# Kernel tuning notes

Measured on AMD Instinct MI355X. Metric: run time of the kernel, lower is better.

The kernel has to match this reference:

```python
import jax, jax.numpy as jnp
import numpy as np

# Static problem sizes (uniform graphs for jit-friendliness)
B = 64          # number of hypergraphs in the batch
N_PER = 32      # shape-nodes per hypergraph (num_nodes_hgraph, uniform)
D_ID = 256      # shape_id_dim
D_MULT = 64     # shape_multiplicity_dim
LATENT = 512    # latent_dim
D_NODE = D_ID + D_MULT           # 320
FEAT = 3 * D_NODE + LATENT       # 1472, MLP input dim
HID = 2 * FEAT                   # 2944
NUM_ATOMS = 11                   # 1 + feature_sizes['num_atoms']
VOCAB_ID, VOCAB_MULT = 100, 20


def setup_inputs() -> dict:
    key = jax.random.key(0)
    ks = jax.random.split(key, 11)
    s1 = 1.0 / np.sqrt(FEAT)
    s2 = 1.0 / np.sqrt(HID)
    s3 = 1.0 / np.sqrt(FEAT)
    return {
        "shape_node_idx": jax.random.randint(ks[0], (B * N_PER,), 0, VOCAB_ID),
        "shape_node_mult": jax.random.randint(ks[1], (B * N_PER,), 0, VOCAB_MULT),
        "z_graph": jax.random.normal(ks[2], (B, LATENT), jnp.float32),
        "id_emb": jax.random.normal(ks[3], (VOCAB_ID, D_ID), jnp.float32) * 0.02,
        "mult_emb": jax.random.normal(ks[4], (VOCAB_MULT, D_MULT), jnp.float32) * 0.02,
        "W1": jax.random.normal(ks[5], (FEAT, HID), jnp.float32) * s1,
        "b1": jnp.zeros((HID,), jnp.float32),
        "W2": jax.random.normal(ks[6], (HID, FEAT), jnp.float32) * s2,
        "b2": jnp.zeros((FEAT,), jnp.float32),
        "W3": jax.random.normal(ks[7], (FEAT, NUM_ATOMS), jnp.float32) * s3,
        "b3": jnp.zeros((NUM_ATOMS,), jnp.float32),
    }


def reference(shape_node_idx, shape_node_mult, z_graph, id_emb, mult_emb,
              W1, b1, W2, b2, W3, b3):
    # Node features: concat of shape-id and multiplicity embeddings -> [B, n, d_node]
    x = jnp.concatenate([id_emb[shape_node_idx], mult_emb[shape_node_mult]], axis=-1)
    x = x.reshape(B, N_PER, D_NODE)

    # Per-graph segment aggregation (node_aggregation='mean') -> [B, d_node]
    agg = x.mean(axis=1)

    # All intra-graph node pairs (block-diagonal edge pattern), edge (i, j):
    # input = [x_i, x_j, z_graph, agg] broadcast to [B, n, n, FEAT]
    xi = jnp.broadcast_to(x[:, :, None, :], (B, N_PER, N_PER, D_NODE))
    xj = jnp.broadcast_to(x[:, None, :, :], (B, N_PER, N_PER, D_NODE))
    zg = jnp.broadcast_to(z_graph[:, None, None, :], (B, N_PER, N_PER, LATENT))
    ag = jnp.broadcast_to(agg[:, None, None, :], (B, N_PER, N_PER, D_NODE))
    feat = jnp.concatenate([xi, xj, zg, ag], axis=-1)  # [B, n, n, FEAT]

    # MLP [FEAT, 2*FEAT, FEAT, NUM_ATOMS] with ReLU activations
    h = jax.nn.relu(jnp.einsum('bijf,fh->bijh', feat, W1) + b1)
    h = jax.nn.relu(jnp.einsum('bijh,hf->bijf', h, W2) + b2)
    logits = jnp.einsum('bijf,fa->bija', h, W3) + b3  # [B, n, n, A]

    # _to_symmetric: average each edge value with its transpose
    logits = 0.5 * (logits + jnp.swapaxes(logits, 1, 2))

    # Flattened per-edge logits (matches sparse COO value order: row-major pairs)
    return logits.reshape(B * N_PER * N_PER, NUM_ATOMS)
```

## Files before the change

### kernel.cpp

```cpp
#include <hip/hip_runtime.h>
#include <stdint.h>

#define NBG   64
#define NPER  32
#define DNODE 320
#define FEAT  1472
#define HIDN  2944
#define FEATP 1536
#define NA    11
#define NROWS 2048
#define MEDGE 65536

typedef __attribute__((ext_vector_type(8))) short    bf16x8;
typedef __attribute__((ext_vector_type(4))) float    fv4;
typedef __attribute__((ext_vector_type(4))) unsigned uiv4;

__device__ __forceinline__ unsigned short f2bf(float f) {
  unsigned u = __builtin_bit_cast(unsigned, f);
  u += 0x7fffu + ((u >> 16) & 1u);
  return (unsigned short)(u >> 16);
}
__device__ __forceinline__ float bf2f(unsigned short h) {
  unsigned u = ((unsigned)h) << 16;
  return __builtin_bit_cast(float, u);
}
__device__ __forceinline__ unsigned cvt_pk_bf16(float lo, float hi) {
  unsigned r;
  asm("v_cvt_pk_bf16_f32 %0, %1, %2" : "=v"(r) : "v"(lo), "v"(hi));
  return r;
}
__device__ __forceinline__ void gload_lds16(const void* g, void* l) {
  __builtin_amdgcn_global_load_lds((const __attribute__((address_space(1))) void*)g,
                                   (__attribute__((address_space(3))) void*)l, 16, 0, 0);
}

__global__ void k_transpose_bf16(const float* __restrict__ src, unsigned short* __restrict__ dst,
                                 int K, int N, int Npad) {
  __shared__ float tile[64][65];
  int k0 = blockIdx.x * 64, n0 = blockIdx.y * 64;
  int r = threadIdx.x >> 2, cb = (threadIdx.x & 3) * 16;
  const float* srow = src + (size_t)(k0 + r) * N + n0 + cb;
#pragma unroll
  for (int c = 0; c < 16; ++c) {
    int n = n0 + cb + c;
    tile[r][cb + c] = (n < N) ? srow[c] : 0.f;
  }
  __syncthreads();
  unsigned short* drow = dst + (size_t)(n0 + r) * K + k0 + cb;
#pragma unroll
  for (int c = 0; c < 16; ++c) drow[c] = f2bf(tile[cb + c][r]);
}

__global__ void k_embed(const int* __restrict__ idx, const int* __restrict__ mlt,
                        const float* __restrict__ id_emb, const float* __restrict__ mult_emb,
                        unsigned short* __restrict__ xb) {
  int t = blockIdx.x, c = threadIdx.x;
  int iv = idx[t], mv = mlt[t];
  xb[t * DNODE + c] = f2bf(id_emb[iv * 256 + c]);
  if (c < 64) xb[t * DNODE + 256 + c] = f2bf(mult_emb[mv * 64 + c]);
}

__global__ void k_agg(const unsigned short* __restrict__ xb, float* __restrict__ agg) {
  int b = blockIdx.x;
  for (int d = threadIdx.x; d < DNODE; d += 256) {
    float s = 0.f;
    for (int i = 0; i < NPER; ++i) s += bf2f(xb[(b * NPER + i) * DNODE + d]);
    agg[b * DNODE + d] = s * (1.f / 32.f);
  }
}

__global__ void k_za(const float* __restrict__ z, const float* __restrict__ agg,
                     unsigned short* __restrict__ za) {
  int b = blockIdx.x;
  for (int c = threadIdx.x; c < 832; c += 256) {
    unsigned short v = 0;
    if (b < NBG) v = (c < 512) ? f2bf(z[b * 512 + c]) : f2bf(agg[b * DNODE + (c - 512)]);
    za[b * 832 + c] = v;
  }
}

__global__ void k_gemm1(const unsigned short* __restrict__ A, int sA, int Mrows,
                        const unsigned short* __restrict__ W1T, int kOff, int Ksteps,
                        float* __restrict__ C, const float* __restrict__ bias) {
  __shared__ alignas(16) unsigned short Als[128 * 32];
  __shared__ alignas(16) unsigned short Bls[128 * 32];
  int bx = blockIdx.x;
  int mt = bx / 23, nc = bx - mt * 23;
  int m0 = mt * 128, n0 = nc * 128;
  int tid = threadIdx.x, lane = tid & 63, w = tid >> 6;

  fv4 acc[4][4] = {};
  for (int kt = 0; kt < Ksteps; ++kt) {
    int k0 = kt * 32;
    __syncthreads();
#pragma unroll
    for (int q = 0; q < 2; ++q) {
      int seg = w * 2 + q;
      int row = seg * 16 + (lane >> 2);
      int col = (lane & 3) * 8;
      gload_lds16(A + (size_t)(m0 + row) * sA + k0 + col, &Als[seg * 512]);
      gload_lds16(W1T + (size_t)(n0 + row) * FEAT + kOff + k0 + col, &Bls[seg * 512]);
    }
    __syncthreads();
    bf16x8 aF[4], bF[4];
#pragma unroll
    for (int mf = 0; mf < 4; ++mf)
      aF[mf] = *(const bf16x8*)&Als[((w >> 1) * 64 + mf * 16 + (lane & 15)) * 32 + (lane >> 4) * 8];
#pragma unroll
    for (int nf = 0; nf < 4; ++nf)
      bF[nf] = *(const bf16x8*)&Bls[((w & 1) * 64 + nf * 16 + (lane & 15)) * 32 + (lane >> 4) * 8];
#pragma unroll
    for (int mf = 0; mf < 4; ++mf)
#pragma unroll
      for (int nf = 0; nf < 4; ++nf)
        acc[mf][nf] = __builtin_amdgcn_mfma_f32_16x16x32_bf16(aF[mf], bF[nf], acc[mf][nf], 0, 0, 0);
  }
  int mq = (w >> 1) * 64, nq = (w & 1) * 64;
#pragma unroll
  for (int mf = 0; mf < 4; ++mf)
#pragma unroll
    for (int nf = 0; nf < 4; ++nf) {
      int n = n0 + nq + nf * 16 + (lane & 15);
      float bv = bias ? bias[n] : 0.f;
#pragma unroll
      for (int r = 0; r < 4; ++r) {
        int m = m0 + mq + mf * 16 + (lane >> 4) * 4 + r;
        if (m < Mrows) C[(size_t)m * HIDN + n] = acc[mf][nf][r] + bv;
      }
    }
}

__global__ void k_pq(float* __restrict__ P1, const float* __restrict__ Q) {
  int r = blockIdx.x;
  const float* q = Q + (size_t)(r >> 5) * HIDN;
  float* p = P1 + (size_t)r * HIDN;
  for (int n = threadIdx.x; n < HIDN; n += 256) p[n] += q[n];
}

__global__ void k_zero(float* __restrict__ p, int n) {
  int i = blockIdx.x * 256 + threadIdx.x;
  if (i < n) p[i] = 0.f;
}

__global__ __launch_bounds__(256, 3)
void k_gemm2(const float* __restrict__ PQ1, const float* __restrict__ P2,
             const unsigned short* __restrict__ W2T,
             const float* __restrict__ b2, const float* __restrict__ W3,
             float* __restrict__ Lraw) {
  __shared__ alignas(16) unsigned char LB[26624];
  int bx = blockIdx.x;
  int mt = bx / 12, nc = bx - mt * 12;
  int m0 = mt * 128, n0 = nc * 128;
  int tid = threadIdx.x, lane = tid & 63, w = tid >> 6;
  int bG = m0 >> 10;
  int i0 = (m0 >> 5) & 31;
  int ks = lane >> 4;
  int r  = lane & 15;

  const int swcolB = ((lane & 3) ^ ((lane >> 3) & 3)) * 8;
  const int swcolP = (((lane >> 1) & 3) ^ ((lane >> 3) & 3)) * 8 + (lane & 1) * 4;

  auto STAGEB = [&](int kt, int buf) {
#pragma unroll
    for (int q = 0; q < 2; ++q) {
      int seg = w * 2 + q;
      int row = seg * 16 + (lane >> 2);
      gload_lds16(W2T + (size_t)(n0 + row) * HIDN + kt * 32 + swcolB,
                  LB + buf * 8192 + seg * 1024);
    }
  };
  auto STAGESRC = [&](int kt, int buf) {
    gload_lds16(P2 + (size_t)(bG * NPER + 8 * w + (lane >> 3)) * HIDN + kt * 32 + swcolP,
                LB + 16384 + buf * 4096 + w * 1024);
    if (w == 0)
      gload_lds16(PQ1 + (size_t)(bG * NPER + i0 + (lane >> 3)) * HIDN + kt * 32 + (lane & 7) * 4,
                  LB + 24576 + buf * 1024);
  };

  fv4 acc[4][4] = {};

  STAGEB(0, 0);
  STAGESRC(0, 0);
  __syncthreads();

  for (int kt = 0; kt < 92; ++kt) {
    int cur = kt & 1, nxt = cur ^ 1;
    if (kt < 91) { STAGEB(kt + 1, nxt); STAGESRC(kt + 1, nxt); }

    const unsigned char* Bb = LB + cur * 8192;
    const unsigned char* Pb = LB + 16384 + cur * 4096;
    const unsigned char* Qb = LB + 24576 + cur * 1024;

    int il0 = (w >> 1) * 2;
    int psw = (ks ^ (r & 3)) * 32;
    fv4 q0[2], q1[2], p0[2], p1[2];
#pragma unroll
    for (int h = 0; h < 2; ++h) {
      q0[h] = *(const fv4*)(Qb + il0 * 128 + ks * 32 + h * 16);
      q1[h] = *(const fv4*)(Qb + (il0 + 1) * 128 + ks * 32 + h * 16);
      p0[h] = *(const fv4*)(Pb + r * 128 + psw + h * 16);
      p1[h] = *(const fv4*)(Pb + (16 + r) * 128 + psw + h * 16);
    }
    bf16x8 bF[4];
#pragma unroll
    for (int nf = 0; nf < 4; ++nf) {
      int brow = (w & 1) * 64 + nf * 16 + r;
      int slot = ks ^ ((brow >> 1) & 3);
      bF[nf] = *(const bf16x8*)(Bb + brow * 64 + slot * 16);
    }

    bf16x8 aF[4];
#pragma unroll
    for (int mf = 0; mf < 4; ++mf) {
      fv4 s0 = (mf & 2 ? q1[0] : q0[0]) + (mf & 1 ? p1[0] : p0[0]);
      fv4 s1 = (mf & 2 ? q1[1] : q0[1]) + (mf & 1 ? p1[1] : p0[1]);
      uiv4 u;
      u[0] = cvt_pk_bf16(fmaxf(s0[0], 0.f), fmaxf(s0[1], 0.f));
      u[1] = cvt_pk_bf16(fmaxf(s0[2], 0.f), fmaxf(s0[3], 0.f));
      u[2] = cvt_pk_bf16(fmaxf(s1[0], 0.f), fmaxf(s1[1], 0.f));
      u[3] = cvt_pk_bf16(fmaxf(s1[2], 0.f), fmaxf(s1[3], 0.f));
      aF[mf] = __builtin_bit_cast(bf16x8, u);
    }

#pragma unroll
    for (int mf = 0; mf < 4; ++mf)
#pragma unroll
      for (int nf = 0; nf < 4; ++nf)
        acc[mf][nf] = __builtin_amdgcn_mfma_f32_16x16x32_bf16(aF[mf], bF[nf], acc[mf][nf], 0, 0, 0);
    __syncthreads();
  }

  float* red = (float*)LB;
  int nq = (w & 1) * 64;
#pragma unroll
  for (int mf = 0; mf < 4; ++mf) {
    float s[4][NA];
#pragma unroll
    for (int rr = 0; rr < 4; ++rr)
#pragma unroll
      for (int a = 0; a < NA; ++a) s[rr][a] = 0.f;
#pragma unroll
    for (int nf = 0; nf < 4; ++nf) {
      int n = n0 + nq + nf * 16 + r;
      if (n < FEAT) {
        float bv = b2[n];
        float w3r[NA];
#pragma unroll
        for (int a = 0; a < NA; ++a) w3r[a] = W3[n * NA + a];
#pragma unroll
        for (int rr = 0; rr < 4; ++rr) {
          float h = fmaxf(acc[mf][nf][rr] + bv, 0.f);
#pragma unroll
          for (int a = 0; a < NA; ++a) s[rr][a] += h * w3r[a];
        }
      }
    }
#pragma unroll
    for (int off = 1; off < 16; off <<= 1)
#pragma unroll
      for (int rr = 0; rr < 4; ++rr)
#pragma unroll
        for (int a = 0; a < NA; ++a) s[rr][a] += __shfl_xor(s[rr][a], off, 64);
    int a = r;
    if (a < NA) {
#pragma unroll
      for (int rr = 0; rr < 4; ++rr)
        red[w * 704 + (mf * 16 + ks * 4 + rr) * NA + a] = s[rr][a];
    }
  }
  __syncthreads();
  for (int e = tid; e < 128 * NA; e += 256) {
    int row = e / NA, a = e - row * NA;
    int wr = row >> 6, rr = row & 63;
    float v = red[(wr * 2 + 0) * 704 + rr * NA + a] + red[(wr * 2 + 1) * 704 + rr * NA + a];
    atomicAdd(&Lraw[(size_t)(m0 + row) * NA + a], v);
  }
}

__global__ void k_sym(const float* __restrict__ Lraw, const float* __restrict__ b3,
                      float* __restrict__ out) {
  int e = blockIdx.x * 256 + threadIdx.x;
  if (e >= MEDGE * NA) return;
  int m = e / NA, a = e - m * NA;
  int msw = (m & ~1023) | ((m & 31) << 5) | ((m >> 5) & 31);
  out[e] = 0.5f * (Lraw[e] + Lraw[(size_t)msw * NA + a]) + b3[a];
}

extern "C" void kernel_launch(void* const* d_in, const int* in_sizes, int n_in,
                              void* d_out, int out_size, void* d_ws, size_t ws_size,
                              hipStream_t stream) {
  const int*   idx      = (const int*)d_in[0];
  const int*   mlt      = (const int*)d_in[1];
  const float* z        = (const float*)d_in[2];
  const float* id_emb   = (const float*)d_in[3];
  const float* mult_emb = (const float*)d_in[4];
  const float* W1       = (const float*)d_in[5];
  const float* b1       = (const float*)d_in[6];
  const float* W2       = (const float*)d_in[7];
  const float* b2       = (const float*)d_in[8];
  const float* W3       = (const float*)d_in[9];
  const float* b3       = (const float*)d_in[10];
  float* out = (float*)d_out;

  uint8_t* ws = (uint8_t*)d_ws;
  size_t o = 0;
  auto alloc = [&](size_t bytes) { size_t r = o; o += (bytes + 255) & ~(size_t)255; return r; };
  size_t oW1T = alloc((size_t)HIDN * FEAT * 2);
  size_t oW2T = alloc((size_t)FEATP * HIDN * 2);
  size_t oXB  = alloc((size_t)NROWS * DNODE * 2);
  size_t oZA  = alloc((size_t)128 * 832 * 2);
  size_t oAG  = alloc((size_t)NBG * DNODE * 4);
  size_t oP1  = alloc((size_t)NROWS * HIDN * 4);
  size_t oP2  = alloc((size_t)NROWS * HIDN * 4);
  size_t oQ   = alloc((size_t)NBG * HIDN * 4);
  size_t oLR  = alloc((size_t)MEDGE * NA * 4);
  if (ws_size < o) return;

  unsigned short* W1T = (unsigned short*)(ws + oW1T);
  unsigned short* W2T = (unsigned short*)(ws + oW2T);
  unsigned short* xb  = (unsigned short*)(ws + oXB);
  unsigned short* za  = (unsigned short*)(ws + oZA);
  float* agg = (float*)(ws + oAG);
  float* P1  = (float*)(ws + oP1);
  float* P2  = (float*)(ws + oP2);
  float* Qm  = (float*)(ws + oQ);
  float* LR  = (float*)(ws + oLR);

  k_transpose_bf16<<<dim3(FEAT / 64, HIDN / 64), 256, 0, stream>>>(W1, W1T, FEAT, HIDN, HIDN);
  k_transpose_bf16<<<dim3(HIDN / 64, FEATP / 64), 256, 0, stream>>>(W2, W2T, HIDN, FEAT, FEATP);
  k_embed<<<NROWS, 256, 0, stream>>>(idx, mlt, id_emb, mult_emb, xb);
  k_agg<<<NBG, 256, 0, stream>>>(xb, agg);
  k_za<<<128, 256, 0, stream>>>(z, agg, za);
  k_gemm1<<<16 * 23, 256, 0, stream>>>(xb, DNODE, NROWS, W1T, 0, 10, P1, nullptr);
  k_gemm1<<<16 * 23, 256, 0, stream>>>(xb, DNODE, NROWS, W1T, 320, 10, P2, nullptr);
  k_gemm1<<<1 * 23, 256, 0, stream>>>(za, 832, NBG, W1T, 640, 26, Qm, b1);
  k_pq<<<NROWS, 256, 0, stream>>>(P1, Qm);
  k_zero<<<(MEDGE * NA + 255) / 256, 256, 0, stream>>>(LR, MEDGE * NA);
  k_gemm2<<<512 * 12, 256, 0, stream>>>(P1, P2, W2T, b2, W3, LR);
  k_sym<<<(MEDGE * NA + 255) / 256, 256, 0, stream>>>(LR, b3, out);
}
```

Before: 1.318 ms.

## Materialize bf16 edge activations and replace atomics with per-column-tile partial sums

Adds a path that precomputes the relu(P1+P2) layer-1 activations for all edges as a bf16 matrix, so the second GEMM streams plain bf16 tiles instead of building them from fp32 sums inside the loop. The atomicAdd reduction is replaced by per-column-tile partial logits, which the symmetrization kernel sums; this also drops the zeroing kernel. The code picks a tier based on available workspace. Materializing the full 65536x2944 bf16 matrix adds a large amount of extra memory traffic, and the partial-sum buffer is twelve times larger than before.

New measurement: 1.317 ms. Within noise of the previous version (-0.0%).

```diff
diff --git a/kernel.cpp b/kernel.cpp
--- a/kernel.cpp
+++ b/kernel.cpp
@@ -142,11 +142,127 @@
   if (i < n) p[i] = 0.f;
 }
 
+__global__ void k_build_A(const float* __restrict__ PQ1, const float* __restrict__ P2,
+                          unsigned short* __restrict__ Abf) {
+  int bi = blockIdx.x;
+  int b = bi >> 5;
+  const float* qrow = PQ1 + (size_t)bi * HIDN;
+  const float* pbase = P2 + (size_t)(b * NPER) * HIDN;
+  unsigned short* abase = Abf + (size_t)bi * NPER * HIDN;
+  for (int j = 0; j < NPER; ++j) {
+    const float* prow = pbase + (size_t)j * HIDN;
+    unsigned short* arow = abase + (size_t)j * HIDN;
+    for (int kc = threadIdx.x; kc < HIDN / 8; kc += 256) {
+      fv4 q0 = *(const fv4*)(qrow + kc * 8);
+      fv4 q1 = *(const fv4*)(qrow + kc * 8 + 4);
+      fv4 p0 = *(const fv4*)(prow + kc * 8);
+      fv4 p1 = *(const fv4*)(prow + kc * 8 + 4);
+      fv4 s0 = q0 + p0, s1 = q1 + p1;
+      uiv4 u;
+      u[0] = cvt_pk_bf16(fmaxf(s0[0], 0.f), fmaxf(s0[1], 0.f));
+      u[1] = cvt_pk_bf16(fmaxf(s0[2], 0.f), fmaxf(s0[3], 0.f));
+      u[2] = cvt_pk_bf16(fmaxf(s1[0], 0.f), fmaxf(s1[1], 0.f));
+      u[3] = cvt_pk_bf16(fmaxf(s1[2], 0.f), fmaxf(s1[3], 0.f));
+      *(uiv4*)(arow + kc * 8) = u;
+    }
+  }
+}
+
+__global__ __launch_bounds__(256, 3)
+void k_gemm2m(const unsigned short* __restrict__ A, const unsigned short* __restrict__ W2T,
+              const float* __restrict__ b2, const float* __restrict__ W3,
+              float* __restrict__ LRp) {
+  __shared__ alignas(16) unsigned char LB[16384];
+  unsigned short* Als = (unsigned short*)LB;
+  unsigned short* Bls = (unsigned short*)(LB + 8192);
+  int raw = blockIdx.x;
+  int bx = (raw & 7) * 768 + (raw >> 3);
+  int mt = bx / 12, nc = bx - mt * 12;
+  int m0 = mt * 128, n0 = nc * 128;
+  int tid = threadIdx.x, lane = tid & 63, w = tid >> 6;
+  int r = lane & 15, ks = lane >> 4;
+
+  fv4 acc[4][4] = {};
+  for (int kt = 0; kt < 92; ++kt) {
+    int k0 = kt * 32;
+    __syncthreads();
+#pragma unroll
+    for (int q = 0; q < 2; ++q) {
+      int seg = w * 2 + q;
+      int row = seg * 16 + (lane >> 2);
+      int col = (lane & 3) * 8;
+      gload_lds16(A + (size_t)(m0 + row) * HIDN + k0 + col, &Als[seg * 512]);
+      gload_lds16(W2T + (size_t)(n0 + row) * HIDN + k0 + col, &Bls[seg * 512]);
+    }
+    __syncthreads();
+    bf16x8 aF[4], bF[4];
+#pragma unroll
+    for (int mf = 0; mf < 4; ++mf)
+      aF[mf] = *(const bf16x8*)&Als[((w >> 1) * 64 + mf * 16 + r) * 32 + ks * 8];
+#pragma unroll
+    for (int nf = 0; nf < 4; ++nf)
+      bF[nf] = *(const bf16x8*)&Bls[((w & 1) * 64 + nf * 16 + r) * 32 + ks * 8];
+#pragma unroll
+    for (int mf = 0; mf < 4; ++mf)
+#pragma unroll
+      for (int nf = 0; nf < 4; ++nf)
+        acc[mf][nf] = __builtin_amdgcn_mfma_f32_16x16x32_bf16(aF[mf], bF[nf], acc[mf][nf], 0, 0, 0);
+  }
+  __syncthreads();
+
+  float* red = (float*)LB;
+  int nq = (w & 1) * 64;
+#pragma unroll
+  for (int mf = 0; mf < 4; ++mf) {
+    float s[4][NA];
+#pragma unroll
+    for (int rr = 0; rr < 4; ++rr)
+#pragma unroll
+      for (int a = 0; a < NA; ++a) s[rr][a] = 0.f;
+#pragma unroll
+    for (int nf = 0; nf < 4; ++nf) {
+      int n = n0 + nq + nf * 16 + r;
+      if (n < FEAT) {
+        float bv = b2[n];
+        float w3r[NA];
+#pragma unroll
+        for (int a = 0; a < NA; ++a) w3r[a] = W3[n * NA + a];
+#pragma unroll
+        for (int rr = 0; rr < 4; ++rr) {
+          float h = fmaxf(acc[mf][nf][rr] + bv, 0.f);
+#pragma unroll
+          for (int a = 0; a < NA; ++a) s[rr][a] += h * w3r[a];
+        }
+      }
+    }
+#pragma unroll
+    for (int off = 1; off < 16; off <<= 1)
+#pragma unroll
+      for (int rr = 0; rr < 4; ++rr)
+#pragma unroll
+        for (int a = 0; a < NA; ++a) s[rr][a] += __shfl_xor(s[rr][a], off, 64);
+    int a = r;
+    if (a < NA) {
+#pragma unroll
+      for (int rr = 0; rr < 4; ++rr)
+        red[w * 704 + (mf * 16 + ks * 4 + rr) * NA + a] = s[rr][a];
+    }
+  }
+  __syncthreads();
+  for (int e = tid; e < 128 * NA; e += 256) {
+    int row = e / NA, a = e - row * NA;
+    int wr = row >> 6, rr = row & 63;
+    float v = red[(wr * 2 + 0) * 704 + rr * NA + a] + red[(wr * 2 + 1) * 704 + rr * NA + a];
+    LRp[(size_t)nc * (MEDGE * NA) + (size_t)(m0 + row) * NA + a] = v;
+  }
+}
+
+template <bool PARTIAL>
 __global__ __launch_bounds__(256, 3)
 void k_gemm2(const float* __restrict__ PQ1, const float* __restrict__ P2,
              const unsigned short* __restrict__ W2T,
              const float* __restrict__ b2, const float* __restrict__ W3,
-             float* __restrict__ Lraw) {
+             float* __restrict__ Lout) {
   __shared__ alignas(16) unsigned char LB[26624];
   int bx = blockIdx.x;
   int mt = bx / 12, nc = bx - mt * 12;
@@ -229,6 +345,7 @@
         acc[mf][nf] = __builtin_amdgcn_mfma_f32_16x16x32_bf16(aF[mf], bF[nf], acc[mf][nf], 0, 0, 0);
     __syncthreads();
   }
+  __syncthreads();
 
   float* red = (float*)LB;
   int nq = (w & 1) * 64;
@@ -273,17 +390,25 @@
     int row = e / NA, a = e - row * NA;
     int wr = row >> 6, rr = row & 63;
     float v = red[(wr * 2 + 0) * 704 + rr * NA + a] + red[(wr * 2 + 1) * 704 + rr * NA + a];
-    atomicAdd(&Lraw[(size_t)(m0 + row) * NA + a], v);
-  }
-}
-
-__global__ void k_sym(const float* __restrict__ Lraw, const float* __restrict__ b3,
+    if (PARTIAL)
+      Lout[(size_t)nc * (MEDGE * NA) + (size_t)(m0 + row) * NA + a] = v;
+    else
+      atomicAdd(&Lout[(size_t)(m0 + row) * NA + a], v);
+  }
+}
+
+template <int NS>
+__global__ void k_sym(const float* __restrict__ LRp, const float* __restrict__ b3,
                       float* __restrict__ out) {
   int e = blockIdx.x * 256 + threadIdx.x;
   if (e >= MEDGE * NA) return;
   int m = e / NA, a = e - m * NA;
   int msw = (m & ~1023) | ((m & 31) << 5) | ((m >> 5) & 31);
-  out[e] = 0.5f * (Lraw[e] + Lraw[(size_t)msw * NA + a]) + b3[a];
+  float s = 0.f;
+#pragma unroll
+  for (int t = 0; t < NS; ++t)
+    s += LRp[(size_t)t * (MEDGE * NA) + e] + LRp[(size_t)t * (MEDGE * NA) + (size_t)msw * NA + a];
+  out[e] = 0.5f * s + b3[a];
 }
 
 extern "C" void kernel_launch(void* const* d_in, const int* in_sizes, int n_in,
@@ -313,8 +438,13 @@
   size_t oP1  = alloc((size_t)NROWS * HIDN * 4);
   size_t oP2  = alloc((size_t)NROWS * HIDN * 4);
   size_t oQ   = alloc((size_t)NBG * HIDN * 4);
-  size_t oLR  = alloc((size_t)MEDGE * NA * 4);
-  if (ws_size < o) return;
+  size_t oLRp = alloc((size_t)12 * MEDGE * NA * 4);
+  size_t needB = o;
+  size_t oA   = alloc((size_t)MEDGE * HIDN * 2);
+  size_t needA = o;
+  size_t needC = oLRp + (((size_t)MEDGE * NA * 4 + 255) & ~(size_t)255);
+  if (ws_size < needC) return;
+  int tier = (ws_size >= needA) ? 0 : (ws_size >= needB ? 1 : 2);
 
   unsigned short* W1T = (unsigned short*)(ws + oW1T);
   unsigned short* W2T = (unsigned short*)(ws + oW2T);
@@ -324,7 +454,8 @@
   float* P1  = (float*)(ws + oP1);
   float* P2  = (float*)(ws + oP2);
   float* Qm  = (float*)(ws + oQ);
-  float* LR  = (float*)(ws + oLR);
+  float* LRp = (float*)(ws + oLRp);
+  unsigned short* Abf = (unsigned short*)(ws + oA);
 
   k_transpose_bf16<<<dim3(FEAT / 64, HIDN / 64), 256, 0, stream>>>(W1, W1T, FEAT, HIDN, HIDN);
   k_transpose_bf16<<<dim3(HIDN / 64, FEATP / 64), 256, 0, stream>>>(W2, W2T, HIDN, FEAT, FEATP);
@@ -335,7 +466,17 @@
   k_gemm1<<<16 * 23, 256, 0, stream>>>(xb, DNODE, NROWS, W1T, 320, 10, P2, nullptr);
   k_gemm1<<<1 * 23, 256, 0, stream>>>(za, 832, NBG, W1T, 640, 26, Qm, b1);
   k_pq<<<NROWS, 256, 0, stream>>>(P1, Qm);
-  k_zero<<<(MEDGE * NA + 255) / 256, 256, 0, stream>>>(LR, MEDGE * NA);
-  k_gemm2<<<512 * 12, 256, 0, stream>>>(P1, P2, W2T, b2, W3, LR);
-  k_sym<<<(MEDGE * NA + 255) / 256, 256, 0, stream>>>(LR, b3, out);
-}
+
+  if (tier == 0) {
+    k_build_A<<<NROWS, 256, 0, stream>>>(P1, P2, Abf);
+    k_gemm2m<<<512 * 12, 256, 0, stream>>>(Abf, W2T, b2, W3, LRp);
+    k_sym<12><<<(MEDGE * NA + 255) / 256, 256, 0, stream>>>(LRp, b3, out);
+  } else if (tier == 1) {
+    k_gemm2<true><<<512 * 12, 256, 0, stream>>>(P1, P2, W2T, b2, W3, LRp);
+    k_sym<12><<<(MEDGE * NA + 255) / 256, 256, 0, stream>>>(LRp, b3, out);
+  } else {
+    k_zero<<<(MEDGE * NA + 255) / 256, 256, 0, stream>>>(LRp, MEDGE * NA);
+    k_gemm2<false><<<512 * 12, 256, 0, stream>>>(P1, P2, W2T, b2, W3, LRp);
+    k_sym<1><<<(MEDGE * NA + 255) / 256, 256, 0, stream>>>(LRp, b3, out);
+  }
+}
```

## Widen gemm2 N-tile to 256, swizzle block order, write partial logits instead of atomics

Applied to the files above, without the earlier changes.

The fused second GEMM now computes 128x256 tiles per block (8 N-fragments per wave), which halves how often the P/Q activation sources are restaged and rebuilt per output column. Block indices are remapped across 8 groups to change the cache locality of co-resident blocks. When the workspace is large enough, each N-chunk writes its partial W3 projection to a separate slice, and the symmetrization kernel sums the six slices, removing the zeroing pass and the atomics. The larger accumulator set raises register and LDS pressure and lowers occupancy to 2 blocks per CU.

Result: faster. 1.154 ms (-12.4%).

```diff
diff --git a/kernel.cpp b/kernel.cpp
--- a/kernel.cpp
+++ b/kernel.cpp
@@ -142,15 +142,17 @@
   if (i < n) p[i] = 0.f;
 }
 
-__global__ __launch_bounds__(256, 3)
+template <bool PARTIAL>
+__global__ __launch_bounds__(256, 2)
 void k_gemm2(const float* __restrict__ PQ1, const float* __restrict__ P2,
              const unsigned short* __restrict__ W2T,
              const float* __restrict__ b2, const float* __restrict__ W3,
-             float* __restrict__ Lraw) {
-  __shared__ alignas(16) unsigned char LB[26624];
-  int bx = blockIdx.x;
-  int mt = bx / 12, nc = bx - mt * 12;
-  int m0 = mt * 128, n0 = nc * 128;
+             float* __restrict__ Lout) {
+  __shared__ alignas(16) unsigned char LB[43008];
+  int raw = blockIdx.x;
+  int bx = (raw & 7) * 384 + (raw >> 3);
+  int mt = bx / 6, nc2 = bx - mt * 6;
+  int m0 = mt * 128, n0 = nc2 * 256;
   int tid = threadIdx.x, lane = tid & 63, w = tid >> 6;
   int bG = m0 >> 10;
   int i0 = (m0 >> 5) & 31;
@@ -162,22 +164,22 @@
 
   auto STAGEB = [&](int kt, int buf) {
 #pragma unroll
-    for (int q = 0; q < 2; ++q) {
-      int seg = w * 2 + q;
+    for (int q = 0; q < 4; ++q) {
+      int seg = w * 4 + q;
       int row = seg * 16 + (lane >> 2);
       gload_lds16(W2T + (size_t)(n0 + row) * HIDN + kt * 32 + swcolB,
-                  LB + buf * 8192 + seg * 1024);
+                  LB + buf * 16384 + seg * 1024);
     }
   };
   auto STAGESRC = [&](int kt, int buf) {
     gload_lds16(P2 + (size_t)(bG * NPER + 8 * w + (lane >> 3)) * HIDN + kt * 32 + swcolP,
-                LB + 16384 + buf * 4096 + w * 1024);
+                LB + 32768 + buf * 4096 + w * 1024);
     if (w == 0)
       gload_lds16(PQ1 + (size_t)(bG * NPER + i0 + (lane >> 3)) * HIDN + kt * 32 + (lane & 7) * 4,
-                  LB + 24576 + buf * 1024);
+                  LB + 40960 + buf * 1024);
   };
 
-  fv4 acc[4][4] = {};
+  fv4 acc[4][8] = {};
 
   STAGEB(0, 0);
   STAGESRC(0, 0);
@@ -187,9 +189,9 @@
     int cur = kt & 1, nxt = cur ^ 1;
     if (kt < 91) { STAGEB(kt + 1, nxt); STAGESRC(kt + 1, nxt); }
 
-    const unsigned char* Bb = LB + cur * 8192;
-    const unsigned char* Pb = LB + 16384 + cur * 4096;
-    const unsigned char* Qb = LB + 24576 + cur * 1024;
+    const unsigned char* Bb = LB + cur * 16384;
+    const unsigned char* Pb = LB + 32768 + cur * 4096;
+    const unsigned char* Qb = LB + 40960 + cur * 1024;
 
     int il0 = (w >> 1) * 2;
     int psw = (ks ^ (r & 3)) * 32;
@@ -201,10 +203,10 @@
       p0[h] = *(const fv4*)(Pb + r * 128 + psw + h * 16);
       p1[h] = *(const fv4*)(Pb + (16 + r) * 128 + psw + h * 16);
     }
-    bf16x8 bF[4];
-#pragma unroll
-    for (int nf = 0; nf < 4; ++nf) {
-      int brow = (w & 1) * 64 + nf * 16 + r;
+    bf16x8 bF[8];
+#pragma unroll
+    for (int nf = 0; nf < 8; ++nf) {
+      int brow = (w & 1) * 128 + nf * 16 + r;
       int slot = ks ^ ((brow >> 1) & 3);
       bF[nf] = *(const bf16x8*)(Bb + brow * 64 + slot * 16);
     }
@@ -223,15 +225,15 @@
     }
 
 #pragma unroll
-    for (int mf = 0; mf < 4; ++mf)
-#pragma unroll
-      for (int nf = 0; nf < 4; ++nf)
+    for (int nf = 0; nf < 8; ++nf)
+#pragma unroll
+      for (int mf = 0; mf < 4; ++mf)
         acc[mf][nf] = __builtin_amdgcn_mfma_f32_16x16x32_bf16(aF[mf], bF[nf], acc[mf][nf], 0, 0, 0);
     __syncthreads();
   }
 
   float* red = (float*)LB;
-  int nq = (w & 1) * 64;
+  int nq = (w & 1) * 128;
 #pragma unroll
   for (int mf = 0; mf < 4; ++mf) {
     float s[4][NA];
@@ -240,7 +242,7 @@
 #pragma unroll
       for (int a = 0; a < NA; ++a) s[rr][a] = 0.f;
 #pragma unroll
-    for (int nf = 0; nf < 4; ++nf) {
+    for (int nf = 0; nf < 8; ++nf) {
       int n = n0 + nq + nf * 16 + r;
       if (n < FEAT) {
         float bv = b2[n];
@@ -273,17 +275,25 @@
     int row = e / NA, a = e - row * NA;
     int wr = row >> 6, rr = row & 63;
     float v = red[(wr * 2 + 0) * 704 + rr * NA + a] + red[(wr * 2 + 1) * 704 + rr * NA + a];
-    atomicAdd(&Lraw[(size_t)(m0 + row) * NA + a], v);
-  }
-}
-
-__global__ void k_sym(const float* __restrict__ Lraw, const float* __restrict__ b3,
+    if (PARTIAL)
+      Lout[(size_t)nc2 * (MEDGE * NA) + (size_t)(m0 + row) * NA + a] = v;
+    else
+      atomicAdd(&Lout[(size_t)(m0 + row) * NA + a], v);
+  }
+}
+
+template <int NS>
+__global__ void k_sym(const float* __restrict__ LRp, const float* __restrict__ b3,
                       float* __restrict__ out) {
   int e = blockIdx.x * 256 + threadIdx.x;
   if (e >= MEDGE * NA) return;
   int m = e / NA, a = e - m * NA;
   int msw = (m & ~1023) | ((m & 31) << 5) | ((m >> 5) & 31);
-  out[e] = 0.5f * (Lraw[e] + Lraw[(size_t)msw * NA + a]) + b3[a];
+  float s = 0.f;
+#pragma unroll
+  for (int t = 0; t < NS; ++t)
+    s += LRp[(size_t)t * (MEDGE * NA) + e] + LRp[(size_t)t * (MEDGE * NA) + (size_t)msw * NA + a];
+  out[e] = 0.5f * s + b3[a];
 }
 
 extern "C" void kernel_launch(void* const* d_in, const int* in_sizes, int n_in,
@@ -313,8 +323,11 @@
   size_t oP1  = alloc((size_t)NROWS * HIDN * 4);
   size_t oP2  = alloc((size_t)NROWS * HIDN * 4);
   size_t oQ   = alloc((size_t)NBG * HIDN * 4);
-  size_t oLR  = alloc((size_t)MEDGE * NA * 4);
-  if (ws_size < o) return;
+  size_t oLRp = alloc((size_t)6 * MEDGE * NA * 4);
+  size_t needPartial = o;
+  size_t needAtomic  = oLRp + (((size_t)MEDGE * NA * 4 + 255) & ~(size_t)255);
+  if (ws_size < needAtomic) return;
+  bool partial = (ws_size >= needPartial);
 
   unsigned short* W1T = (unsigned short*)(ws + oW1T);
   unsigned short* W2T = (unsigned short*)(ws + oW2T);
@@ -324,7 +337,7 @@
   float* P1  = (float*)(ws + oP1);
   float* P2  = (float*)(ws + oP2);
   float* Qm  = (float*)(ws + oQ);
-  float* LR  = (float*)(ws + oLR);
+  float* LRp = (float*)(ws + oLRp);
 
   k_transpose_bf16<<<dim3(FEAT / 64, HIDN / 64), 256, 0, stream>>>(W1, W1T, FEAT, HIDN, HIDN);
   k_transpose_bf16<<<dim3(HIDN / 64, FEATP / 64), 256, 0, stream>>>(W2, W2T, HIDN, FEAT, FEATP);
@@ -335,7 +348,13 @@
   k_gemm1<<<16 * 23, 256, 0, stream>>>(xb, DNODE, NROWS, W1T, 320, 10, P2, nullptr);
   k_gemm1<<<1 * 23, 256, 0, stream>>>(za, 832, NBG, W1T, 640, 26, Qm, b1);
   k_pq<<<NROWS, 256, 0, stream>>>(P1, Qm);
-  k_zero<<<(MEDGE * NA + 255) / 256, 256, 0, stream>>>(LR, MEDGE * NA);
-  k_gemm2<<<512 * 12, 256, 0, stream>>>(P1, P2, W2T, b2, W3, LR);
-  k_sym<<<(MEDGE * NA + 255) / 256, 256, 0, stream>>>(LR, b3, out);
-}
+
+  if (partial) {
+    k_gemm2<true><<<512 * 6, 256, 0, stream>>>(P1, P2, W2T, b2, W3, LRp);
+    k_sym<6><<<(MEDGE * NA + 255) / 256, 256, 0, stream>>>(LRp, b3, out);
+  } else {
+    k_zero<<<(MEDGE * NA + 255) / 256, 256, 0, stream>>>(LRp, MEDGE * NA);
+    k_gemm2<false><<<512 * 6, 256, 0, stream>>>(P1, P2, W2T, b2, W3, LRp);
+    k_sym<1><<<(MEDGE * NA + 255) / 256, 256, 0, stream>>>(LRp, b3, out);
+  }
+}
```

## Make gemm2 blocks persistent over all N chunks, dropping atomics and zero pass

Applied to the files above, without the earlier changes.

Each gemm2 block now owns one 128-row M tile and loops over all six 256-wide N chunks, accumulating the W3 projection in shared memory. Final logits are written directly, so the zero kernel and global atomicAdd are gone. P/Q sources are now read straight from global memory rather than staged in LDS. Block ids are remapped so concurrent blocks share W2T chunks. The grid drops from 6144 to 512 blocks with larger tiles and two waves per SIMD, which lowers occupancy and may leave CUs idle or add latency from the unstaged global loads.

New measurement: 1.594 ms. 1.21x slower.

```diff
diff --git a/kernel.cpp b/kernel.cpp
--- a/kernel.cpp
+++ b/kernel.cpp
@@ -137,74 +137,70 @@
   for (int n = threadIdx.x; n < HIDN; n += 256) p[n] += q[n];
 }
 
-__global__ void k_zero(float* __restrict__ p, int n) {
-  int i = blockIdx.x * 256 + threadIdx.x;
-  if (i < n) p[i] = 0.f;
-}
-
-__global__ __launch_bounds__(256, 3)
+__global__ __launch_bounds__(256, 2)
 void k_gemm2(const float* __restrict__ PQ1, const float* __restrict__ P2,
              const unsigned short* __restrict__ W2T,
              const float* __restrict__ b2, const float* __restrict__ W3,
              float* __restrict__ Lraw) {
-  __shared__ alignas(16) unsigned char LB[26624];
-  int bx = blockIdx.x;
-  int mt = bx / 12, nc = bx - mt * 12;
-  int m0 = mt * 128, n0 = nc * 128;
+  __shared__ alignas(16) unsigned char LB[44032];
+  int raw = blockIdx.x;
+  int mt = (raw & 7) * 64 + (raw >> 3);
+  int m0 = mt * 128;
   int tid = threadIdx.x, lane = tid & 63, w = tid >> 6;
   int bG = m0 >> 10;
   int i0 = (m0 >> 5) & 31;
   int ks = lane >> 4;
   int r  = lane & 15;
+  int il0 = (w >> 1) * 2;
 
   const int swcolB = ((lane & 3) ^ ((lane >> 3) & 3)) * 8;
-  const int swcolP = (((lane >> 1) & 3) ^ ((lane >> 3) & 3)) * 8 + (lane & 1) * 4;
-
-  auto STAGEB = [&](int kt, int buf) {
-#pragma unroll
-    for (int q = 0; q < 2; ++q) {
-      int seg = w * 2 + q;
+
+  const float* p0g = P2 + (size_t)(bG * NPER + r) * HIDN + ks * 8;
+  const float* p1g = p0g + (size_t)16 * HIDN;
+  const float* q0g = PQ1 + (size_t)(bG * NPER + i0 + il0) * HIDN + ks * 8;
+  const float* q1g = q0g + HIDN;
+
+  float* wred = (float*)(LB + 32768);
+  for (int e = tid; e < 4 * 704; e += 256) wred[e] = 0.f;
+
+  auto STAGEB = [&](int nc, int kt, int buf) {
+#pragma unroll
+    for (int q = 0; q < 4; ++q) {
+      int seg = w * 4 + q;
       int row = seg * 16 + (lane >> 2);
-      gload_lds16(W2T + (size_t)(n0 + row) * HIDN + kt * 32 + swcolB,
-                  LB + buf * 8192 + seg * 1024);
+      gload_lds16(W2T + (size_t)(nc * 256 + row) * HIDN + kt * 32 + swcolB,
+                  LB + buf * 16384 + seg * 1024);
     }
   };
-  auto STAGESRC = [&](int kt, int buf) {
-    gload_lds16(P2 + (size_t)(bG * NPER + 8 * w + (lane >> 3)) * HIDN + kt * 32 + swcolP,
-                LB + 16384 + buf * 4096 + w * 1024);
-    if (w == 0)
-      gload_lds16(PQ1 + (size_t)(bG * NPER + i0 + (lane >> 3)) * HIDN + kt * 32 + (lane & 7) * 4,
-                  LB + 24576 + buf * 1024);
-  };
-
-  fv4 acc[4][4] = {};
-
-  STAGEB(0, 0);
-  STAGESRC(0, 0);
+
+  fv4 acc[4][8] = {};
+  STAGEB(0, 0, 0);
   __syncthreads();
 
-  for (int kt = 0; kt < 92; ++kt) {
-    int cur = kt & 1, nxt = cur ^ 1;
-    if (kt < 91) { STAGEB(kt + 1, nxt); STAGESRC(kt + 1, nxt); }
-
-    const unsigned char* Bb = LB + cur * 8192;
-    const unsigned char* Pb = LB + 16384 + cur * 4096;
-    const unsigned char* Qb = LB + 24576 + cur * 1024;
-
-    int il0 = (w >> 1) * 2;
-    int psw = (ks ^ (r & 3)) * 32;
+  int nc_c = 0, kt_c = 0;
+  for (int s = 0; s < 552; ++s) {
+    int cur = s & 1;
+    if (s < 551) {
+      int kt_s = kt_c + 1, nc_s = nc_c;
+      if (kt_s == 92) { kt_s = 0; ++nc_s; }
+      STAGEB(nc_s, kt_s, cur ^ 1);
+    }
+
+    const unsigned char* Bb = LB + cur * 16384;
+    int ko = kt_c * 32;
+
     fv4 q0[2], q1[2], p0[2], p1[2];
 #pragma unroll
     for (int h = 0; h < 2; ++h) {
-      q0[h] = *(const fv4*)(Qb + il0 * 128 + ks * 32 + h * 16);
-      q1[h] = *(const fv4*)(Qb + (il0 + 1) * 128 + ks * 32 + h * 16);
-      p0[h] = *(const fv4*)(Pb + r * 128 + psw + h * 16);
-      p1[h] = *(const fv4*)(Pb + (16 + r) * 128 + psw + h * 16);
-    }
-    bf16x8 bF[4];
-#pragma unroll
-    for (int nf = 0; nf < 4; ++nf) {
-      int brow = (w & 1) * 64 + nf * 16 + r;
+      q0[h] = *(const fv4*)(q0g + ko + h * 4);
+      q1[h] = *(const fv4*)(q1g + ko + h * 4);
+      p0[h] = *(const fv4*)(p0g + ko + h * 4);
+      p1[h] = *(const fv4*)(p1g + ko + h * 4);
+    }
+    bf16x8 bF[8];
+#pragma unroll
+    for (int nf = 0; nf < 8; ++nf) {
+      int brow = (w & 1) * 128 + nf * 16 + r;
       int slot = ks ^ ((brow >> 1) & 3);
       bF[nf] = *(const bf16x8*)(Bb + brow * 64 + slot * 16);
     }
@@ -223,57 +219,64 @@
     }
 
 #pragma unroll
-    for (int mf = 0; mf < 4; ++mf)
-#pragma unroll
-      for (int nf = 0; nf < 4; ++nf)
+    for (int nf = 0; nf < 8; ++nf)
+#pragma unroll
+      for (int mf = 0; mf < 4; ++mf)
         acc[mf][nf] = __builtin_amdgcn_mfma_f32_16x16x32_bf16(aF[mf], bF[nf], acc[mf][nf], 0, 0, 0);
-    __syncthreads();
-  }
-
-  float* red = (float*)LB;
-  int nq = (w & 1) * 64;
-#pragma unroll
-  for (int mf = 0; mf < 4; ++mf) {
-    float s[4][NA];
-#pragma unroll
-    for (int rr = 0; rr < 4; ++rr)
-#pragma unroll
-      for (int a = 0; a < NA; ++a) s[rr][a] = 0.f;
-#pragma unroll
-    for (int nf = 0; nf < 4; ++nf) {
-      int n = n0 + nq + nf * 16 + r;
-      if (n < FEAT) {
-        float bv = b2[n];
-        float w3r[NA];
-#pragma unroll
-        for (int a = 0; a < NA; ++a) w3r[a] = W3[n * NA + a];
-#pragma unroll
-        for (int rr = 0; rr < 4; ++rr) {
-          float h = fmaxf(acc[mf][nf][rr] + bv, 0.f);
-#pragma unroll
-          for (int a = 0; a < NA; ++a) s[rr][a] += h * w3r[a];
+
+    if (kt_c == 91) {
+      int nq = (w & 1) * 128;
+#pragma unroll
+      for (int mf = 0; mf < 4; ++mf) {
+        float sv[4][NA];
+#pragma unroll
+        for (int rr = 0; rr < 4; ++rr)
+#pragma unroll
+          for (int a = 0; a < NA; ++a) sv[rr][a] = 0.f;
+#pragma unroll
+        for (int nf = 0; nf < 8; ++nf) {
+          int n = nc_c * 256 + nq + nf * 16 + r;
+          if (n < FEAT) {
+            float bv = b2[n];
+            float w3r[NA];
+#pragma unroll
+            for (int a = 0; a < NA; ++a) w3r[a] = W3[n * NA + a];
+#pragma unroll
+            for (int rr = 0; rr < 4; ++rr) {
+              float h = fmaxf(acc[mf][nf][rr] + bv, 0.f);
+#pragma unroll
+              for (int a = 0; a < NA; ++a) sv[rr][a] += h * w3r[a];
+            }
+          }
+        }
+#pragma unroll
+        for (int off = 1; off < 16; off <<= 1)
+#pragma unroll
+          for (int rr = 0; rr < 4; ++rr)
+#pragma unroll
+            for (int a = 0; a < NA; ++a) sv[rr][a] += __shfl_xor(sv[rr][a], off, 64);
+        int a = r;
+        if (a < NA) {
+#pragma unroll
+          for (int rr = 0; rr < 4; ++rr)
+            wred[w * 704 + (mf * 16 + ks * 4 + rr) * NA + a] += sv[rr][a];
         }
       }
-    }
-#pragma unroll
-    for (int off = 1; off < 16; off <<= 1)
-#pragma unroll
-      for (int rr = 0; rr < 4; ++rr)
-#pragma unroll
-        for (int a = 0; a < NA; ++a) s[rr][a] += __shfl_xor(s[rr][a], off, 64);
-    int a = r;
-    if (a < NA) {
-#pragma unroll
-      for (int rr = 0; rr < 4; ++rr)
-        red[w * 704 + (mf * 16 + ks * 4 + rr) * NA + a] = s[rr][a];
-    }
-  }
-  __syncthreads();
+#pragma unroll
+      for (int mf = 0; mf < 4; ++mf)
+#pragma unroll
+        for (int nf = 0; nf < 8; ++nf)
+          acc[mf][nf] = fv4{0.f, 0.f, 0.f, 0.f};
+    }
+    __syncthreads();
+    if (++kt_c == 92) { kt_c = 0; ++nc_c; }
+  }
+
   for (int e = tid; e < 128 * NA; e += 256) {
     int row = e / NA, a = e - row * NA;
     int wr = row >> 6, rr = row & 63;
-    float v = red[(wr * 2 + 0) * 704 + rr * NA + a] + red[(wr * 2 + 1) * 704 + rr * NA + a];
-    atomicAdd(&Lraw[(size_t)(m0 + row) * NA + a], v);
+    float v = wred[(wr * 2 + 0) * 704 + rr * NA + a] + wred[(wr * 2 + 1) * 704 + rr * NA + a];
+    Lraw[(size_t)(m0 + row) * NA + a] = v;
   }
 }
 
@@ -335,7 +338,6 @@
   k_gemm1<<<16 * 23, 256, 0, stream>>>(xb, DNODE, NROWS, W1T, 320, 10, P2, nullptr);
   k_gemm1<<<1 * 23, 256, 0, stream>>>(za, 832, NBG, W1T, 640, 26, Qm, b1);
   k_pq<<<NROWS, 256, 0, stream>>>(P1, Qm);
-  k_zero<<<(MEDGE * NA + 255) / 256, 256, 0, stream>>>(LR, MEDGE * NA);
-  k_gemm2<<<512 * 12, 256, 0, stream>>>(P1, P2, W2T, b2, W3, LR);
+  k_gemm2<<<512, 256, 0, stream>>>(P1, P2, W2T, b2, W3, LR);
   k_sym<<<(MEDGE * NA + 255) / 256, 256, 0, stream>>>(LR, b3, out);
 }
```
